# Optimization experiments

Measured on AMD Instinct MI355X. Metric: run time of the kernel, lower is better.

Reference implementation:

```python
import jax, jax.numpy as jnp
import numpy as np

N_NODES = 100000
N_EDGES = 3200000
N_GRAPHS = 128
HID = 64


def gcn_conv(x, src, dst, W, b, n_nodes):
    # PyG GCNConv: add self-loops, symmetric normalization, scatter-add aggregate
    loop = jnp.arange(n_nodes, dtype=src.dtype)
    s = jnp.concatenate([src, loop])
    d = jnp.concatenate([dst, loop])
    deg = jax.ops.segment_sum(jnp.ones_like(d, dtype=x.dtype), d, num_segments=n_nodes)
    dinv = jnp.where(deg > 0, jax.lax.rsqrt(deg), 0.0)
    norm = dinv[s] * dinv[d]                      # [E+N]
    h = x @ W                                     # [N, out] small GEMM first
    msg = h[s] * norm[:, None]                    # [E+N, out] gather + scale
    out = jax.ops.segment_sum(msg, d, num_segments=n_nodes)
    return out + b


def setup_inputs() -> dict:
    key = jax.random.key(0)
    ks = jax.random.split(key, 9)
    x = jax.random.normal(ks[0], (N_NODES, 2), dtype=jnp.float32)
    edge_index = jax.random.randint(ks[1], (2, N_EDGES), 0, N_NODES, dtype=jnp.int64 if jax.config.jax_enable_x64 else jnp.int32)
    batch = jnp.sort(jax.random.randint(ks[2], (N_NODES,), 0, N_GRAPHS, dtype=edge_index.dtype))
    W1 = jax.random.normal(ks[3], (2, HID), dtype=jnp.float32) / jnp.sqrt(2.0)
    b1 = jax.random.normal(ks[4], (HID,), dtype=jnp.float32) * 0.01
    W2 = jax.random.normal(ks[5], (HID, HID), dtype=jnp.float32) / jnp.sqrt(float(HID))
    b2 = jax.random.normal(ks[6], (HID,), dtype=jnp.float32) * 0.01
    Wfc = jax.random.normal(ks[7], (HID, 1), dtype=jnp.float32) / jnp.sqrt(float(HID))
    bfc = jax.random.normal(ks[8], (1,), dtype=jnp.float32) * 0.01
    return {"x": x, "edge_index": edge_index, "batch": batch,
            "W1": W1, "b1": b1, "W2": W2, "b2": b2, "Wfc": Wfc, "bfc": bfc}


def reference(x, edge_index, batch, W1, b1, W2, b2, Wfc, bfc):
    src, dst = edge_index[0], edge_index[1]
    h = jax.nn.relu(gcn_conv(x, src, dst, W1, b1, N_NODES))
    h = jax.nn.relu(gcn_conv(h, src, dst, W2, b2, N_NODES))
    # global mean pool over graphs
    sums = jax.ops.segment_sum(h, batch, num_segments=N_GRAPHS)
    cnts = jax.ops.segment_sum(jnp.ones((N_NODES,), dtype=h.dtype), batch, num_segments=N_GRAPHS)
    pooled = sums / jnp.maximum(cnts, 1.0)[:, None]   # [G, HID]
    return pooled @ Wfc + bfc                          # [G, 1]
```

## Files before the change

### kernel.cpp

```cpp
#include <hip/hip_runtime.h>

constexpr int N  = 100000;
constexpr int E  = 3200000;
constexpr int G  = 128;
constexpr int H  = 64;

__global__ __launch_bounds__(256) void k_count(const int* __restrict__ dst,
                                               int* __restrict__ cnt) {
    int e = blockIdx.x * 256 + threadIdx.x;
    if (e < E) atomicAdd(&cnt[dst[e]], 1);
}

__global__ __launch_bounds__(256) void k_dinv(const float* __restrict__ x,
                                              const int* __restrict__ cnt,
                                              float* __restrict__ dinv,
                                              float2* __restrict__ gx) {
    int v = blockIdx.x * 256 + threadIdx.x;
    if (v < N) {
        float d = rsqrtf((float)(cnt[v] + 1));
        dinv[v] = d;
        float2 xv = ((const float2*)x)[v];
        gx[v] = make_float2(xv.x * d, xv.y * d);
    }
}

__global__ __launch_bounds__(1024) void k_scan(const int* __restrict__ cnt,
                                               int* __restrict__ offs,
                                               int* __restrict__ cursor) {
    constexpr int T = 1024;
    constexpr int PER = (N + T - 1) / T;
    int tid = threadIdx.x;
    int begin = tid * PER;
    int end = begin + PER; if (end > N) end = N;

    int total = 0;
    for (int i = begin; i < end; ++i) total += cnt[i];

    __shared__ int wsum[16];
    int lane = tid & 63, wid = tid >> 6;
    int incl = total;
    #pragma unroll
    for (int off = 1; off < 64; off <<= 1) {
        int t = __shfl_up(incl, off);
        if (lane >= off) incl += t;
    }
    if (lane == 63) wsum[wid] = incl;
    __syncthreads();
    if (wid == 0 && lane < 16) {
        int w = wsum[lane];
        #pragma unroll
        for (int off = 1; off < 16; off <<= 1) {
            int t = __shfl_up(w, off);
            if (lane >= off) w += t;
        }
        wsum[lane] = w;
    }
    __syncthreads();
    int waveBase = (wid == 0) ? 0 : wsum[wid - 1];
    int run = waveBase + (incl - total);
    for (int i = begin; i < end; ++i) {
        offs[i] = run;
        cursor[i] = run;
        run += cnt[i];
    }
}

__global__ __launch_bounds__(256) void k_fill(const int* __restrict__ src,
                                              const int* __restrict__ dst,
                                              int* __restrict__ cursor,
                                              int* __restrict__ csr) {
    int e = blockIdx.x * 256 + threadIdx.x;
    if (e < E) {
        int d = dst[e];
        int pos = atomicAdd(&cursor[d], 1);
        csr[pos] = src[e];
    }
}

__global__ __launch_bounds__(256) void k_agg1(const int* __restrict__ csr,
                                              const int* __restrict__ offs,
                                              const int* __restrict__ cnt,
                                              const float* __restrict__ dinv,
                                              const float2* __restrict__ gx,
                                              float2* __restrict__ aggx) {
    int lane = threadIdx.x & 63;
    int v = (blockIdx.x * 256 + threadIdx.x) >> 6;
    if (v >= N) return;
    int start = offs[v], dg = cnt[v];
    float ax = 0.f, ay = 0.f;
    for (int i = lane; i < dg; i += 64) {
        int s = csr[start + i];
        float2 g = gx[s];
        ax += g.x; ay += g.y;
    }
    #pragma unroll
    for (int off = 1; off < 64; off <<= 1) {
        ax += __shfl_xor(ax, off);
        ay += __shfl_xor(ay, off);
    }
    if (lane == 0) {
        float d = dinv[v];
        float2 g = gx[v];
        aggx[v] = make_float2(d * (ax + g.x), d * (ay + g.y));
    }
}

__global__ __launch_bounds__(256) void k_mlp(const float2* __restrict__ aggx,
                                             const float* __restrict__ W1,
                                             const float* __restrict__ b1,
                                             const float* __restrict__ W2,
                                             const float* __restrict__ dinv,
                                             float* __restrict__ g2) {
    int lane = threadIdx.x & 63;
    int wave = (blockIdx.x * 256 + threadIdx.x) >> 6;
    int nw = gridDim.x * 4;

    float w2col[64];
    #pragma unroll
    for (int k = 0; k < 64; ++k) w2col[k] = W2[k * 64 + lane];
    float w10 = W1[lane], w11 = W1[64 + lane], bb = b1[lane];

    for (int v = wave; v < N; v += nw) {
        float2 a = aggx[v];
        float tt = fmaxf(fmaf(a.y, w11, fmaf(a.x, w10, bb)), 0.f);
        float a0 = 0.f, a1 = 0.f, a2 = 0.f, a3 = 0.f;
        #pragma unroll
        for (int k = 0; k < 64; k += 4) {
            float t0 = __int_as_float(__builtin_amdgcn_readlane(__float_as_int(tt), k + 0));
            float t1 = __int_as_float(__builtin_amdgcn_readlane(__float_as_int(tt), k + 1));
            float t2 = __int_as_float(__builtin_amdgcn_readlane(__float_as_int(tt), k + 2));
            float t3 = __int_as_float(__builtin_amdgcn_readlane(__float_as_int(tt), k + 3));
            a0 = fmaf(t0, w2col[k + 0], a0);
            a1 = fmaf(t1, w2col[k + 1], a1);
            a2 = fmaf(t2, w2col[k + 2], a2);
            a3 = fmaf(t3, w2col[k + 3], a3);
        }
        g2[(size_t)v * 64 + lane] = ((a0 + a1) + (a2 + a3)) * dinv[v];
    }
}

__global__ __launch_bounds__(256) void k_agg2(const int* __restrict__ csr,
                                              const int* __restrict__ offs,
                                              const int* __restrict__ cnt,
                                              const float* __restrict__ dinv,
                                              const float* __restrict__ b2,
                                              const float* __restrict__ g2,
                                              const int* __restrict__ batch,
                                              float* __restrict__ pooled,
                                              int* __restrict__ cntg) {
    int lane = threadIdx.x & 63;
    int v = (blockIdx.x * 256 + threadIdx.x) >> 6;
    if (v >= N) return;
    int start = offs[v], dg = cnt[v];
    float acc = g2[(size_t)v * 64 + lane];

    int base = 0;
    while (base < dg) {
        int chunk = dg - base; if (chunk > 64) chunk = 64;
        int idx = csr[start + base + lane];
        int i = 0;
        for (; i + 8 <= chunk; i += 8) {
            const float* r0 = g2 + (size_t)__builtin_amdgcn_readlane(idx, i + 0) * 64;
            const float* r1 = g2 + (size_t)__builtin_amdgcn_readlane(idx, i + 1) * 64;
            const float* r2 = g2 + (size_t)__builtin_amdgcn_readlane(idx, i + 2) * 64;
            const float* r3 = g2 + (size_t)__builtin_amdgcn_readlane(idx, i + 3) * 64;
            const float* r4 = g2 + (size_t)__builtin_amdgcn_readlane(idx, i + 4) * 64;
            const float* r5 = g2 + (size_t)__builtin_amdgcn_readlane(idx, i + 5) * 64;
            const float* r6 = g2 + (size_t)__builtin_amdgcn_readlane(idx, i + 6) * 64;
            const float* r7 = g2 + (size_t)__builtin_amdgcn_readlane(idx, i + 7) * 64;
            float f0 = r0[lane], f1 = r1[lane], f2 = r2[lane], f3 = r3[lane];
            float f4 = r4[lane], f5 = r5[lane], f6 = r6[lane], f7 = r7[lane];
            acc += ((f0 + f1) + (f2 + f3)) + ((f4 + f5) + (f6 + f7));
        }
        for (; i < chunk; ++i) {
            const float* r = g2 + (size_t)__builtin_amdgcn_readlane(idx, i) * 64;
            acc += r[lane];
        }
        base += chunk;
    }

    float o = fmaxf(fmaf(dinv[v], acc, b2[lane]), 0.f);
    int b = batch[v];
    atomicAdd(&pooled[b * 64 + lane], o);
    if (lane == 0) atomicAdd(&cntg[b], 1);
}

__global__ __launch_bounds__(64) void k_final(const float* __restrict__ pooled,
                                              const int* __restrict__ cntg,
                                              const float* __restrict__ Wfc,
                                              const float* __restrict__ bfc,
                                              float* __restrict__ out) {
    int g = blockIdx.x;
    int j = threadIdx.x;
    float c = fmaxf((float)cntg[g], 1.f);
    float p = (pooled[g * 64 + j] / c) * Wfc[j];
    #pragma unroll
    for (int off = 32; off >= 1; off >>= 1) p += __shfl_down(p, off);
    if (j == 0) out[g] = p + bfc[0];
}

extern "C" void kernel_launch(void* const* d_in, const int* in_sizes, int n_in,
                              void* d_out, int out_size, void* d_ws, size_t ws_size,
                              hipStream_t stream) {
    const float* x     = (const float*)d_in[0];
    const int*   edge  = (const int*)d_in[1];
    const int*   batch = (const int*)d_in[2];
    const float* W1    = (const float*)d_in[3];
    const float* b1    = (const float*)d_in[4];
    const float* W2    = (const float*)d_in[5];
    const float* b2    = (const float*)d_in[6];
    const float* Wfc   = (const float*)d_in[7];
    const float* bfc   = (const float*)d_in[8];
    float* out = (float*)d_out;

    const int* src = edge;
    const int* dst = edge + E;

    char* base = (char*)d_ws;
    size_t o = 0;
    auto alloc = [&](size_t bytes) -> void* {
        void* p = base + o;
        o += (bytes + 1023) & ~size_t(1023);
        return p;
    };
    int*    cnt    = (int*)alloc((size_t)N * 4);
    float*  dinv   = (float*)alloc((size_t)N * 4);
    float2* gx     = (float2*)alloc((size_t)N * 8);
    float2* aggx   = (float2*)alloc((size_t)N * 8);
    int*    offs   = (int*)alloc((size_t)N * 4);
    int*    cursor = (int*)alloc((size_t)N * 4);
    int*    csr    = (int*)alloc((size_t)E * 4 + 1024);
    float*  g2     = (float*)alloc((size_t)N * H * 4);
    float*  pooled = (float*)alloc((size_t)G * H * 4);
    int*    cntg   = (int*)alloc((size_t)G * 4);

    hipMemsetAsync(cnt, 0, (size_t)N * 4, stream);
    hipMemsetAsync(pooled, 0, (size_t)G * H * 4, stream);
    hipMemsetAsync(cntg, 0, (size_t)G * 4, stream);

    k_count<<<(E + 255) / 256, 256, 0, stream>>>(dst, cnt);
    k_dinv<<<(N + 255) / 256, 256, 0, stream>>>(x, cnt, dinv, gx);
    k_scan<<<1, 1024, 0, stream>>>(cnt, offs, cursor);
    k_fill<<<(E + 255) / 256, 256, 0, stream>>>(src, dst, cursor, csr);
    k_agg1<<<(N + 3) / 4, 256, 0, stream>>>(csr, offs, cnt, dinv, gx, aggx);
    k_mlp<<<1024, 256, 0, stream>>>(aggx, W1, b1, W2, dinv, g2);
    k_agg2<<<(N + 3) / 4, 256, 0, stream>>>(csr, offs, cnt, dinv, b2, g2, batch, pooled, cntg);
    k_final<<<G, 64, 0, stream>>>(pooled, cntg, Wfc, bfc, out);
}
```

Before: 1.340 ms.

## Split layer-2 features into column slabs and aggregate slab-by-slab for cache locality

```diff
diff --git a/kernel.cpp b/kernel.cpp
--- a/kernel.cpp
+++ b/kernel.cpp
@@ -4,6 +4,8 @@
 constexpr int E  = 3200000;
 constexpr int G  = 128;
 constexpr int H  = 64;
+constexpr int NP = 8;
+constexpr int CP = H / NP;
 
 __global__ __launch_bounds__(256) void k_count(const int* __restrict__ dst,
                                                int* __restrict__ cnt) {
@@ -110,7 +112,7 @@
                                              const float* __restrict__ b1,
                                              const float* __restrict__ W2,
                                              const float* __restrict__ dinv,
-                                             float* __restrict__ g2) {
+                                             float* __restrict__ g2s) {
     int lane = threadIdx.x & 63;
     int wave = (blockIdx.x * 256 + threadIdx.x) >> 6;
     int nw = gridDim.x * 4;
@@ -119,6 +121,8 @@
     #pragma unroll
     for (int k = 0; k < 64; ++k) w2col[k] = W2[k * 64 + lane];
     float w10 = W1[lane], w11 = W1[64 + lane], bb = b1[lane];
+
+    size_t soff = (size_t)(lane >> 3) * ((size_t)N * CP) + (size_t)(lane & 7);
 
     for (int v = wave; v < N; v += nw) {
         float2 a = aggx[v];
@@ -135,54 +139,55 @@
             a2 = fmaf(t2, w2col[k + 2], a2);
             a3 = fmaf(t3, w2col[k + 3], a3);
         }
-        g2[(size_t)v * 64 + lane] = ((a0 + a1) + (a2 + a3)) * dinv[v];
-    }
-}
-
-__global__ __launch_bounds__(256) void k_agg2(const int* __restrict__ csr,
-                                              const int* __restrict__ offs,
-                                              const int* __restrict__ cnt,
-                                              const float* __restrict__ dinv,
-                                              const float* __restrict__ b2,
-                                              const float* __restrict__ g2,
-                                              const int* __restrict__ batch,
-                                              float* __restrict__ pooled,
-                                              int* __restrict__ cntg) {
+        g2s[soff + (size_t)v * CP] = ((a0 + a1) + (a2 + a3)) * dinv[v];
+    }
+}
+
+__global__ __launch_bounds__(256) void k_agg2s(const int* __restrict__ csr,
+                                               const int* __restrict__ offs,
+                                               const int* __restrict__ cnt,
+                                               const float* __restrict__ dinv,
+                                               const float* __restrict__ b2p,
+                                               const float* __restrict__ tab,
+                                               const int* __restrict__ batch,
+                                               float* __restrict__ pooledp,
+                                               int* __restrict__ cntg,
+                                               int do_cnt) {
     int lane = threadIdx.x & 63;
     int v = (blockIdx.x * 256 + threadIdx.x) >> 6;
     if (v >= N) return;
+    int es = lane >> 3;
+    int ch = lane & 7;
     int start = offs[v], dg = cnt[v];
-    float acc = g2[(size_t)v * 64 + lane];
-
+
+    float acc = 0.f;
     int base = 0;
     while (base < dg) {
-        int chunk = dg - base; if (chunk > 64) chunk = 64;
-        int idx = csr[start + base + lane];
-        int i = 0;
-        for (; i + 8 <= chunk; i += 8) {
-            const float* r0 = g2 + (size_t)__builtin_amdgcn_readlane(idx, i + 0) * 64;
-            const float* r1 = g2 + (size_t)__builtin_amdgcn_readlane(idx, i + 1) * 64;
-            const float* r2 = g2 + (size_t)__builtin_amdgcn_readlane(idx, i + 2) * 64;
-            const float* r3 = g2 + (size_t)__builtin_amdgcn_readlane(idx, i + 3) * 64;
-            const float* r4 = g2 + (size_t)__builtin_amdgcn_readlane(idx, i + 4) * 64;
-            const float* r5 = g2 + (size_t)__builtin_amdgcn_readlane(idx, i + 5) * 64;
-            const float* r6 = g2 + (size_t)__builtin_amdgcn_readlane(idx, i + 6) * 64;
-            const float* r7 = g2 + (size_t)__builtin_amdgcn_readlane(idx, i + 7) * 64;
-            float f0 = r0[lane], f1 = r1[lane], f2 = r2[lane], f3 = r3[lane];
-            float f4 = r4[lane], f5 = r5[lane], f6 = r6[lane], f7 = r7[lane];
-            acc += ((f0 + f1) + (f2 + f3)) + ((f4 + f5) + (f6 + f7));
+        #pragma unroll
+        for (int it = 0; it < 8; ++it) {
+            int e0 = base + it * 8;
+            if (e0 >= dg) break;
+            int e = e0 + es;
+            bool ok = e < dg;
+            int ec = ok ? e : (dg - 1);
+            int row = csr[start + ec];
+            float val = tab[(size_t)row * CP + ch];
+            acc += ok ? val : 0.f;
         }
-        for (; i < chunk; ++i) {
-            const float* r = g2 + (size_t)__builtin_amdgcn_readlane(idx, i) * 64;
-            acc += r[lane];
-        }
-        base += chunk;
-    }
-
-    float o = fmaxf(fmaf(dinv[v], acc, b2[lane]), 0.f);
-    int b = batch[v];
-    atomicAdd(&pooled[b * 64 + lane], o);
-    if (lane == 0) atomicAdd(&cntg[b], 1);
+        base += 64;
+    }
+
+    acc += __shfl_xor(acc, 8);
+    acc += __shfl_xor(acc, 16);
+    acc += __shfl_xor(acc, 32);
+
+    if (lane < 8) {
+        acc += tab[(size_t)v * CP + ch];
+        float o = fmaxf(fmaf(dinv[v], acc, b2p[ch]), 0.f);
+        int b = batch[v];
+        atomicAdd(&pooledp[b * 64 + ch], o);
+        if (do_cnt && lane == 0) atomicAdd(&cntg[b], 1);
+    }
 }
 
 __global__ __launch_bounds__(64) void k_final(const float* __restrict__ pooled,
@@ -230,7 +235,7 @@
     int*    offs   = (int*)alloc((size_t)N * 4);
     int*    cursor = (int*)alloc((size_t)N * 4);
     int*    csr    = (int*)alloc((size_t)E * 4 + 1024);
-    float*  g2     = (float*)alloc((size_t)N * H * 4);
+    float*  g2s    = (float*)alloc((size_t)N * H * 4);
     float*  pooled = (float*)alloc((size_t)G * H * 4);
     int*    cntg   = (int*)alloc((size_t)G * 4);
 
@@ -243,7 +248,12 @@
     k_scan<<<1, 1024, 0, stream>>>(cnt, offs, cursor);
     k_fill<<<(E + 255) / 256, 256, 0, stream>>>(src, dst, cursor, csr);
     k_agg1<<<(N + 3) / 4, 256, 0, stream>>>(csr, offs, cnt, dinv, gx, aggx);
-    k_mlp<<<1024, 256, 0, stream>>>(aggx, W1, b1, W2, dinv, g2);
-    k_agg2<<<(N + 3) / 4, 256, 0, stream>>>(csr, offs, cnt, dinv, b2, g2, batch, pooled, cntg);
+    k_mlp<<<1024, 256, 0, stream>>>(aggx, W1, b1, W2, dinv, g2s);
+    for (int p = 0; p < NP; ++p) {
+        k_agg2s<<<(N + 3) / 4, 256, 0, stream>>>(
+            csr, offs, cnt, dinv, b2 + p * CP,
+            g2s + (size_t)p * N * CP, batch,
+            pooled + p * CP, cntg, p == 0 ? 1 : 0);
+    }
     k_final<<<G, 64, 0, stream>>>(pooled, cntg, Wfc, bfc, out);
 }
```

New measurement: 1.897 ms. 1.42x slower.
